# Performance work log

Measured on AMD Instinct MI355X. Metric: run time of the kernel, lower is better.

## Reference

```python
import jax, jax.numpy as jnp
import numpy as np

NUM_CLASSES = 64
BASE_MARGIN = 0.1
ADAPTIVE_WEIGHT = 0.1
STAT_WEIGHT = 0.1


def setup_inputs() -> dict:
    key = jax.random.key(0)
    k1, k2 = jax.random.split(key)
    feats = jax.random.normal(k1, (4096, 512), dtype=jnp.float32)
    labels = jax.random.randint(k2, (4096,), 0, NUM_CLASSES, dtype=jnp.int64)
    return {"feats": feats, "labels": labels}


def _forward(feats, labels):
    N, D = feats.shape
    # pairwise euclidean distances (torch.cdist p=2), nan-safe sqrt
    sq = jnp.sum(feats * feats, axis=-1)                      # [N]
    d2 = sq[:, None] + sq[None, :] - 2.0 * (feats @ feats.T)  # [N,N]
    d2 = jnp.maximum(d2, 0.0)
    dist = jnp.sqrt(jnp.where(d2 > 0.0, d2, 1.0))
    dist = jnp.where(d2 > 0.0, dist, 0.0)

    # class stats (first-call EMA == batch stats), under stop_gradient (torch.no_grad)
    sg = jax.lax.stop_gradient(feats)
    counts = jax.ops.segment_sum(jnp.ones((N,), feats.dtype), labels, NUM_CLASSES)  # [C]
    denom = jnp.maximum(counts, 1.0)[:, None]
    cmean = jax.ops.segment_sum(sg, labels, NUM_CLASSES) / denom                    # [C,D]
    cmsq = jax.ops.segment_sum(sg * sg, labels, NUM_CLASSES) / denom                # [C,D]
    cvar = jnp.maximum(cmsq - cmean * cmean, 0.0)  # biased variance (unbiased=False)

    # statistical margin per sample: ||f_i - mean[y_i]|| * mean(var[y_i])
    diff = feats - cmean[labels]                               # grads flow via feats only
    center_dist2 = jnp.sum(diff * diff, axis=-1)
    center_dist = jnp.sqrt(jnp.where(center_dist2 > 0.0, center_dist2, 1.0))
    center_dist = jnp.where(center_dist2 > 0.0, center_dist, 0.0)
    uncertainty = jnp.mean(cvar, axis=-1)[labels]              # [N]
    stat_margin = center_dist * uncertainty

    same = labels[:, None] == labels[None, :]                  # [N,N]
    eye = jnp.eye(N, dtype=bool)
    pos_mask = same & ~eye                                     # matches pos_dist > 0 filter
    neg_mask = ~same

    big = jnp.asarray(1e30, dist.dtype)
    hardest_pos = jnp.max(jnp.where(pos_mask, dist, -big), axis=1)
    hardest_neg = jnp.min(jnp.where(neg_mask, dist, big), axis=1)
    pos_cnt = jnp.sum(pos_mask, axis=1).astype(dist.dtype)
    neg_cnt = jnp.sum(neg_mask, axis=1).astype(dist.dtype)
    mean_pos = jnp.sum(jnp.where(pos_mask, dist, 0.0), axis=1) / jnp.maximum(pos_cnt, 1.0)
    mean_neg = jnp.sum(jnp.where(neg_mask, dist, 0.0), axis=1) / jnp.maximum(neg_cnt, 1.0)

    final_margin = (BASE_MARGIN + ADAPTIVE_WEIGHT * (mean_neg - mean_pos)
                    + STAT_WEIGHT * stat_margin)
    per_sample = jax.nn.relu(hardest_pos - hardest_neg + final_margin)

    valid = (pos_cnt > 0) & (neg_cnt > 0)
    n_valid = jnp.sum(valid.astype(dist.dtype))
    loss = jnp.sum(jnp.where(valid, per_sample, 0.0)) / jnp.maximum(n_valid, 1.0)
    return jnp.where(n_valid > 0, loss, 0.0)


def reference(feats, labels):
    return _forward(feats, labels)
```

## Files before the change

### kernel.cpp

```cpp
#include <hip/hip_runtime.h>
#include <hip/hip_bf16.h>


#define NN 4096
#define DD 512
#define NCLS 64

typedef __bf16 bf16x8 __attribute__((ext_vector_type(8)));
typedef float f32x4 __attribute__((ext_vector_type(4)));

__device__ __forceinline__ void gload_lds16(const void* g, void* l) {
  __builtin_amdgcn_global_load_lds(
      (const __attribute__((address_space(1))) void*)g,
      (__attribute__((address_space(3))) void*)l, 16, 0, 0);
}

__global__ __launch_bounds__(512) void k_stats(
    const float* __restrict__ feats, const int* __restrict__ labels,
    float* __restrict__ counts, float* __restrict__ cmean,
    float* __restrict__ pvar) {
  __shared__ __align__(16) int slab[NN];
  __shared__ int list[NN];
  __shared__ int chunk_off[64];
  __shared__ int sM;
  __shared__ float red1[512], red2[512];
  const int c = blockIdx.x >> 2;
  const int part = blockIdx.x & 3;
  const int t = threadIdx.x;
  const int lane = t & 63;
  const int wv = t >> 6;
  for (int i = t; i < NN; i += 512) slab[i] = labels[i];
  __syncthreads();
  for (int ch = wv; ch < 64; ch += 8) {
    const unsigned long long m = __ballot(slab[ch * 64 + lane] == c);
    if (lane == 0) chunk_off[ch] = __popcll(m);
  }
  __syncthreads();
  if (wv == 0) {
    const int v = chunk_off[lane];
    int inc = v;
#pragma unroll
    for (int off = 1; off < 64; off <<= 1) {
      const int o = __shfl_up(inc, off);
      if (lane >= off) inc += o;
    }
    chunk_off[lane] = inc - v;
    if (lane == 63) sM = inc;
  }
  __syncthreads();
  const int M = sM;
  for (int ch = wv; ch < 64; ch += 8) {
    const bool my = (slab[ch * 64 + lane] == c);
    const unsigned long long m = __ballot(my);
    if (my) {
      const int pos = chunk_off[ch] + __popcll(m & ((1ULL << lane) - 1ULL));
      list[pos] = ch * 64 + lane;
    }
  }
  __syncthreads();
  const int d = (part << 7) + (t & 127);
  const int sub = t >> 7;
  float s1 = 0.f, s2 = 0.f;
  int m = sub;
  for (; m + 16 <= M; m += 16) {
    float v[4];
#pragma unroll
    for (int e = 0; e < 4; ++e) v[e] = feats[(size_t)list[m + 4 * e] * DD + d];
#pragma unroll
    for (int e = 0; e < 4; ++e) { s1 += v[e]; s2 += v[e] * v[e]; }
  }
  for (; m < M; m += 4) {
    const float v = feats[(size_t)list[m] * DD + d];
    s1 += v; s2 += v * v;
  }
  red1[t] = s1;
  red2[t] = s2;
  __syncthreads();
  float var = 0.f;
  if (t < 128) {
    const float a1 = red1[t] + red1[t + 128] + red1[t + 256] + red1[t + 384];
    const float a2 = red2[t] + red2[t + 128] + red2[t + 256] + red2[t + 384];
    const float den = fmaxf((float)M, 1.f);
    const float mean = a1 / den;
    var = fmaxf(a2 / den - mean * mean, 0.f);
    cmean[c * DD + d] = mean;
  }
  __syncthreads();
  if (t < 128) red1[t] = var;
  __syncthreads();
  for (int s = 64; s > 0; s >>= 1) {
    if (t < s) red1[t] += red1[t + s];
    __syncthreads();
  }
  if (t == 0) {
    pvar[(c << 2) + part] = red1[0];
    if (part == 0) counts[c] = (float)M;
  }
}

__global__ __launch_bounds__(256) void k_row(
    const float* __restrict__ feats, const int* __restrict__ labels,
    const float* __restrict__ cmean, unsigned short* __restrict__ fb,
    float* __restrict__ sqb, float* __restrict__ cd2) {
  const int w = threadIdx.x >> 6;
  const int lane = threadIdx.x & 63;
  const int row = blockIdx.x * 4 + w;
  const int lab = labels[row];
  const float4* fr = (const float4*)(feats + (size_t)row * DD);
  const float4* cm = (const float4*)(cmean + (size_t)lab * DD);
  float sq = 0.f, c2 = 0.f;
  unsigned int ob[4];
#pragma unroll
  for (int h = 0; h < 2; ++h) {
    const float4 f = fr[lane * 2 + h];
    const float4 cv = cm[lane * 2 + h];
    const float fe[4] = {f.x, f.y, f.z, f.w};
    const float ce[4] = {cv.x, cv.y, cv.z, cv.w};
    unsigned short us[4];
#pragma unroll
    for (int e = 0; e < 4; ++e) {
      const __bf16 b = (__bf16)fe[e];
      const float bf = (float)b;
      sq += bf * bf;
      const float dd = fe[e] - ce[e];
      c2 += dd * dd;
      us[e] = __builtin_bit_cast(unsigned short, b);
    }
    ob[h * 2]     = (unsigned int)us[0] | ((unsigned int)us[1] << 16);
    ob[h * 2 + 1] = (unsigned int)us[2] | ((unsigned int)us[3] << 16);
  }
  *(uint4*)(fb + (size_t)row * DD + lane * 8) = make_uint4(ob[0], ob[1], ob[2], ob[3]);
#pragma unroll
  for (int off = 32; off > 0; off >>= 1) {
    sq += __shfl_xor(sq, off);
    c2 += __shfl_xor(c2, off);
  }
  if (lane == 0) {
    sqb[row] = sq;
    cd2[row] = c2;
  }
}

__global__ __launch_bounds__(512, 2) void k_gemm(
    const unsigned short* __restrict__ fb, const float* __restrict__ sqb,
    const int* __restrict__ labels,
    float* __restrict__ php, float* __restrict__ phn,
    float* __restrict__ pst, float* __restrict__ pss) {
  __shared__ __align__(16) unsigned short sA[2][256 * 64];
  __shared__ __align__(16) unsigned short sB[2][256 * 64];
  __shared__ int s_labi[256], s_labj[256];
  __shared__ float s_sqi[256], s_sqj[256];

  const int bid = blockIdx.x;
  const int xcd = bid & 7;
  const int w8 = bid >> 3;
  const int ib = ((xcd & 3) << 2) + (w8 & 3);
  const int jb = ((xcd >> 2) << 3) + (w8 >> 2);
  const int ibase = ib << 8, jbase = jb << 8;
  const int t = threadIdx.x;
  const int lane = t & 63;
  const int w = t >> 6;
  const int wm = w >> 2;
  const int wn = w & 3;
  const int rin = lane & 15;
  const int g4 = lane >> 4;
  const int swzbyte = (g4 ^ (rin & 7)) << 4;
  const int abase = ((wm << 7) + rin) << 7;
  const int bbase = ((wn << 6) + rin) << 7;

  if (t < 256) {
    s_labi[t] = labels[ibase + t];
    s_labj[t] = labels[jbase + t];
    s_sqi[t] = sqb[ibase + t];
    s_sqj[t] = sqb[jbase + t];
  }

  const unsigned short* gA[4];
  const unsigned short* gB[4];
  int lo[4];
#pragma unroll
  for (int r = 0; r < 4; ++r) {
    const int q = (r << 9) + t;
    const int row = q >> 3;
    const int ch = q & 7;
    const int koff = (ch ^ (row & 7)) << 3;
    gA[r] = fb + (size_t)(ibase + row) * DD + koff;
    gB[r] = fb + (size_t)(jbase + row) * DD + koff;
    lo[r] = q << 3;
  }

  f32x4 acc[8][4];
#pragma unroll
  for (int mi = 0; mi < 8; ++mi)
#pragma unroll
    for (int nj = 0; nj < 4; ++nj)
      acc[mi][nj] = (f32x4){0.f, 0.f, 0.f, 0.f};

#pragma unroll
  for (int r = 0; r < 4; ++r) {
    gload_lds16(gA[r], &sA[0][lo[r]]);
    gload_lds16(gB[r], &sB[0][lo[r]]);
  }

#pragma unroll
  for (int kt = 0; kt < 8; ++kt) {
    const int cur = kt & 1;
    if (kt < 7) {
#pragma unroll
      for (int r = 0; r < 4; ++r) {
        gload_lds16(gA[r] + ((kt + 1) << 6), &sA[cur ^ 1][lo[r]]);
        gload_lds16(gB[r] + ((kt + 1) << 6), &sB[cur ^ 1][lo[r]]);
      }
      asm volatile("s_waitcnt vmcnt(8)" ::: "memory");
    } else {
      asm volatile("s_waitcnt vmcnt(0)" ::: "memory");
    }
    __builtin_amdgcn_s_barrier();
    const char* A = (const char*)sA[cur];
    const char* B = (const char*)sB[cur];
#pragma unroll
    for (int ks = 0; ks < 2; ++ks) {
      bf16x8 af[8], bg[4];
#pragma unroll
      for (int mi = 0; mi < 8; ++mi)
        af[mi] = *(const bf16x8*)(A + abase + (mi << 11) + (swzbyte ^ (ks << 6)));
#pragma unroll
      for (int nj = 0; nj < 4; ++nj)
        bg[nj] = *(const bf16x8*)(B + bbase + (nj << 11) + (swzbyte ^ (ks << 6)));
#pragma unroll
      for (int mi = 0; mi < 8; ++mi)
#pragma unroll
        for (int nj = 0; nj < 4; ++nj)
          acc[mi][nj] = __builtin_amdgcn_mfma_f32_16x16x32_bf16(
              af[mi], bg[nj], acc[mi][nj], 0, 0, 0);
    }
    if (kt < 7) {
      asm volatile("s_waitcnt lgkmcnt(0)" ::: "memory");
      __builtin_amdgcn_s_barrier();
    }
  }

  float qj[4];
  int lj[4];
#pragma unroll
  for (int nj = 0; nj < 4; ++nj) {
    const int cl = (wn << 6) + (nj << 4) + rin;
    qj[nj] = s_sqj[cl];
    lj[nj] = s_labj[cl];
  }
  const int jidx = (jb << 2) + wn;
#pragma unroll
  for (int mi = 0; mi < 8; ++mi) {
#pragma unroll
    for (int r = 0; r < 4; ++r) {
      const int rl = (wm << 7) + (mi << 4) + (g4 << 2) + r;
      const float qi = s_sqi[rl];
      const int li = s_labi[rl];
      float hp = 0.f, hn = 1e30f, st = 0.f, ss = 0.f;
#pragma unroll
      for (int nj = 0; nj < 4; ++nj) {
        const float g = acc[mi][nj][r];
        float d2 = qi + qj[nj] - 2.f * g;
        d2 = fmaxf(d2, 0.f);
        const float dist = sqrtf(d2);
        const bool same = (li == lj[nj]);
        const float dp = same ? dist : 0.f;
        hp = fmaxf(hp, dp);
        hn = fminf(hn, same ? 1e30f : dist);
        st += dist;
        ss += dp;
      }
#pragma unroll
      for (int off = 1; off < 16; off <<= 1) {
        hp = fmaxf(hp, __shfl_xor(hp, off));
        hn = fminf(hn, __shfl_xor(hn, off));
        st += __shfl_xor(st, off);
        ss += __shfl_xor(ss, off);
      }
      if (rin == 0) {
        const int grow = ibase + rl;
        php[jidx * NN + grow] = hp;
        phn[jidx * NN + grow] = hn;
        pst[jidx * NN + grow] = st;
        pss[jidx * NN + grow] = ss;
      }
    }
  }
}

__global__ __launch_bounds__(1024) void k_fin1(
    const int* __restrict__ labels, const float* __restrict__ counts,
    const float* __restrict__ pvar, const float* __restrict__ cd2,
    const float* __restrict__ php, const float* __restrict__ phn,
    const float* __restrict__ pst, const float* __restrict__ pss,
    float* __restrict__ pf) {
  const int t = threadIdx.x;
  const int wv = t >> 6;
  const int lane = t & 63;
  const int row = blockIdx.x * 16 + wv;
  const size_t idx = (size_t)lane * NN + row;
  float hp = php[idx];
  float hn = phn[idx];
  float st = pst[idx];
  float ss = pss[idx];
#pragma unroll
  for (int off = 1; off < 64; off <<= 1) {
    hp = fmaxf(hp, __shfl_xor(hp, off));
    hn = fminf(hn, __shfl_xor(hn, off));
    st += __shfl_xor(st, off);
    ss += __shfl_xor(ss, off);
  }
  __shared__ float r1[16], r2[16];
  if (lane == 0) {
    const int lab = labels[row];
    const float cnt = counts[lab];
    const float pos = cnt - 1.f;
    const float neg = (float)NN - cnt;
    const float mean_pos = ss / fmaxf(pos, 1.f);
    const float mean_neg = (st - ss) / fmaxf(neg, 1.f);
    const float c2 = cd2[row];
    const float cdist = (c2 > 0.f) ? sqrtf(c2) : 0.f;
    const float uncert = (pvar[lab * 4] + pvar[lab * 4 + 1] +
                          pvar[lab * 4 + 2] + pvar[lab * 4 + 3]) * (1.f / 512.f);
    const float margin = 0.1f + 0.1f * (mean_neg - mean_pos) + 0.1f * (cdist * uncert);
    const float ps = fmaxf(hp - hn + margin, 0.f);
    const bool valid = (pos > 0.f) && (neg > 0.f);
    r1[wv] = valid ? ps : 0.f;
    r2[wv] = valid ? 1.f : 0.f;
  }
  __syncthreads();
  if (t == 0) {
    float s = 0.f, c = 0.f;
#pragma unroll
    for (int k = 0; k < 16; ++k) { s += r1[k]; c += r2[k]; }
    pf[2 * blockIdx.x] = s;
    pf[2 * blockIdx.x + 1] = c;
  }
}

__global__ __launch_bounds__(256) void k_fin2(const float* __restrict__ pf,
                                              float* __restrict__ out) {
  const int t = threadIdx.x;
  const int lane = t & 63;
  const int w = t >> 6;
  float s = pf[2 * t];
  float c = pf[2 * t + 1];
#pragma unroll
  for (int off = 1; off < 64; off <<= 1) {
    s += __shfl_xor(s, off);
    c += __shfl_xor(c, off);
  }
  __shared__ float ws1[4], ws2[4];
  if (lane == 0) { ws1[w] = s; ws2[w] = c; }
  __syncthreads();
  if (t == 0) {
    s = ws1[0] + ws1[1] + ws1[2] + ws1[3];
    c = ws2[0] + ws2[1] + ws2[2] + ws2[3];
    out[0] = (c > 0.f) ? (s / fmaxf(c, 1.f)) : 0.f;
  }
}

extern "C" void kernel_launch(void* const* d_in, const int* in_sizes, int n_in,
                              void* d_out, int out_size, void* d_ws, size_t ws_size,
                              hipStream_t stream) {
  (void)in_sizes; (void)n_in; (void)out_size; (void)ws_size;
  const float* feats = (const float*)d_in[0];
  const int* labels = (const int*)d_in[1];
  char* w = (char*)d_ws;
  float* counts = (float*)(w + 0);
  float* pvar   = (float*)(w + 1024);
  float* sqb    = (float*)(w + 2048);
  float* cd2    = (float*)(w + 18432);
  float* pf     = (float*)(w + 34816);
  float* cmean  = (float*)(w + 36864);
  unsigned short* fb = (unsigned short*)(w + 167936);
  float* php = (float*)(w + 4362240);
  float* phn = (float*)(w + 5410816);
  float* pst = (float*)(w + 6459392);
  float* pss = (float*)(w + 7507968);

  k_stats<<<dim3(256), dim3(512), 0, stream>>>(feats, labels, counts, cmean, pvar);
  k_row<<<dim3(1024), dim3(256), 0, stream>>>(feats, labels, cmean, fb, sqb, cd2);
  k_gemm<<<dim3(256), dim3(512), 0, stream>>>(fb, sqb, labels, php, phn, pst, pss);
  k_fin1<<<dim3(256), dim3(1024), 0, stream>>>(labels, counts, pvar, cd2,
                                               php, phn, pst, pss, pf);
  k_fin2<<<dim3(1), dim3(256), 0, stream>>>(pf, (float*)d_out);
}
```

Before: 58.36 us.

## Retile distance GEMM to 128x256 tiles with 4 waves and K-step 32

The pairwise-distance GEMM now uses 128x256 output tiles computed by 256-thread blocks (4 waves) instead of 256x256 tiles with 512 threads. The launch grows to 512 blocks, and the K loop runs 16 steps of 32 with a new LDS swizzle. A dummy LDS pad array is added, apparently to shape shared-memory usage and occupancy. The intent is to spread work over more blocks per CU and shrink per-block LDS. In exchange, each block reuses the B tile less and synchronises twice as often in the K loop.

New measurement: 60.56 us. 3.8% more time.

```diff
diff --git a/kernel.cpp b/kernel.cpp
--- a/kernel.cpp
+++ b/kernel.cpp
@@ -141,52 +141,61 @@
   }
 }
 
-__global__ __launch_bounds__(512, 2) void k_gemm(
+__global__ __launch_bounds__(256, 2) void k_gemm(
     const unsigned short* __restrict__ fb, const float* __restrict__ sqb,
     const int* __restrict__ labels,
     float* __restrict__ php, float* __restrict__ phn,
     float* __restrict__ pst, float* __restrict__ pss) {
-  __shared__ __align__(16) unsigned short sA[2][256 * 64];
-  __shared__ __align__(16) unsigned short sB[2][256 * 64];
-  __shared__ int s_labi[256], s_labj[256];
-  __shared__ float s_sqi[256], s_sqj[256];
+  __shared__ __align__(16) unsigned short sA[2][128 * 32];
+  __shared__ __align__(16) unsigned short sB[2][256 * 32];
+  __shared__ int s_labi[128], s_labj[256];
+  __shared__ float s_sqi[128], s_sqj[256];
+  __shared__ float s_pad[1024];
 
   const int bid = blockIdx.x;
   const int xcd = bid & 7;
   const int w8 = bid >> 3;
-  const int ib = ((xcd & 3) << 2) + (w8 & 3);
-  const int jb = ((xcd >> 2) << 3) + (w8 >> 2);
-  const int ibase = ib << 8, jbase = jb << 8;
+  const int ib = ((xcd & 3) << 3) + (w8 & 7);
+  const int jb = ((xcd >> 2) << 3) + (w8 >> 3);
+  const int ibase = ib << 7, jbase = jb << 8;
   const int t = threadIdx.x;
   const int lane = t & 63;
-  const int w = t >> 6;
-  const int wm = w >> 2;
-  const int wn = w & 3;
+  const int wn = t >> 6;
   const int rin = lane & 15;
   const int g4 = lane >> 4;
-  const int swzbyte = (g4 ^ (rin & 7)) << 4;
-  const int abase = ((wm << 7) + rin) << 7;
-  const int bbase = ((wn << 6) + rin) << 7;
-
-  if (t < 256) {
+  if (s_labj[0] == 0x7fffffff) s_pad[0] = 1.f;
+  const int koffr = (g4 ^ ((rin >> 1) & 3)) << 4;
+  const int bbase = ((wn << 6) + rin) << 6;
+
+  if (t < 128) {
     s_labi[t] = labels[ibase + t];
+    s_sqi[t] = sqb[ibase + t];
+  }
+  {
     s_labj[t] = labels[jbase + t];
-    s_sqi[t] = sqb[ibase + t];
     s_sqj[t] = sqb[jbase + t];
   }
 
-  const unsigned short* gA[4];
+  const unsigned short* gA[2];
   const unsigned short* gB[4];
-  int lo[4];
+  int loA[2], loB[4];
+#pragma unroll
+  for (int r = 0; r < 2; ++r) {
+    const int q = (r << 8) + t;
+    const int row = q >> 2;
+    const int ch = q & 3;
+    const int koff = (ch ^ ((row >> 1) & 3)) << 3;
+    gA[r] = fb + (size_t)(ibase + row) * DD + koff;
+    loA[r] = q << 3;
+  }
 #pragma unroll
   for (int r = 0; r < 4; ++r) {
-    const int q = (r << 9) + t;
-    const int row = q >> 3;
-    const int ch = q & 7;
-    const int koff = (ch ^ (row & 7)) << 3;
-    gA[r] = fb + (size_t)(ibase + row) * DD + koff;
+    const int q = (r << 8) + t;
+    const int row = q >> 2;
+    const int ch = q & 3;
+    const int koff = (ch ^ ((row >> 1) & 3)) << 3;
     gB[r] = fb + (size_t)(jbase + row) * DD + koff;
-    lo[r] = q << 3;
+    loB[r] = q << 3;
   }
 
   f32x4 acc[8][4];
@@ -197,44 +206,40 @@
       acc[mi][nj] = (f32x4){0.f, 0.f, 0.f, 0.f};
 
 #pragma unroll
-  for (int r = 0; r < 4; ++r) {
-    gload_lds16(gA[r], &sA[0][lo[r]]);
-    gload_lds16(gB[r], &sB[0][lo[r]]);
-  }
-
-#pragma unroll
-  for (int kt = 0; kt < 8; ++kt) {
+  for (int r = 0; r < 2; ++r) gload_lds16(gA[r], &sA[0][loA[r]]);
+#pragma unroll
+  for (int r = 0; r < 4; ++r) gload_lds16(gB[r], &sB[0][loB[r]]);
+
+#pragma unroll
+  for (int kt = 0; kt < 16; ++kt) {
     const int cur = kt & 1;
-    if (kt < 7) {
-#pragma unroll
-      for (int r = 0; r < 4; ++r) {
-        gload_lds16(gA[r] + ((kt + 1) << 6), &sA[cur ^ 1][lo[r]]);
-        gload_lds16(gB[r] + ((kt + 1) << 6), &sB[cur ^ 1][lo[r]]);
-      }
-      asm volatile("s_waitcnt vmcnt(8)" ::: "memory");
+    if (kt < 15) {
+      const int nk = (kt + 1) << 5;
+#pragma unroll
+      for (int r = 0; r < 2; ++r) gload_lds16(gA[r] + nk, &sA[cur ^ 1][loA[r]]);
+#pragma unroll
+      for (int r = 0; r < 4; ++r) gload_lds16(gB[r] + nk, &sB[cur ^ 1][loB[r]]);
+      asm volatile("s_waitcnt vmcnt(6)" ::: "memory");
     } else {
       asm volatile("s_waitcnt vmcnt(0)" ::: "memory");
     }
     __builtin_amdgcn_s_barrier();
     const char* A = (const char*)sA[cur];
     const char* B = (const char*)sB[cur];
-#pragma unroll
-    for (int ks = 0; ks < 2; ++ks) {
-      bf16x8 af[8], bg[4];
-#pragma unroll
-      for (int mi = 0; mi < 8; ++mi)
-        af[mi] = *(const bf16x8*)(A + abase + (mi << 11) + (swzbyte ^ (ks << 6)));
+    bf16x8 af[8], bg[4];
+#pragma unroll
+    for (int mi = 0; mi < 8; ++mi)
+      af[mi] = *(const bf16x8*)(A + (((mi << 4) + rin) << 6) + koffr);
+#pragma unroll
+    for (int nj = 0; nj < 4; ++nj)
+      bg[nj] = *(const bf16x8*)(B + bbase + (nj << 10) + koffr);
+#pragma unroll
+    for (int mi = 0; mi < 8; ++mi)
 #pragma unroll
       for (int nj = 0; nj < 4; ++nj)
-        bg[nj] = *(const bf16x8*)(B + bbase + (nj << 11) + (swzbyte ^ (ks << 6)));
-#pragma unroll
-      for (int mi = 0; mi < 8; ++mi)
-#pragma unroll
-        for (int nj = 0; nj < 4; ++nj)
-          acc[mi][nj] = __builtin_amdgcn_mfma_f32_16x16x32_bf16(
-              af[mi], bg[nj], acc[mi][nj], 0, 0, 0);
-    }
-    if (kt < 7) {
+        acc[mi][nj] = __builtin_amdgcn_mfma_f32_16x16x32_bf16(
+            af[mi], bg[nj], acc[mi][nj], 0, 0, 0);
+    if (kt < 15) {
       asm volatile("s_waitcnt lgkmcnt(0)" ::: "memory");
       __builtin_amdgcn_s_barrier();
     }
@@ -253,7 +258,7 @@
   for (int mi = 0; mi < 8; ++mi) {
 #pragma unroll
     for (int r = 0; r < 4; ++r) {
-      const int rl = (wm << 7) + (mi << 4) + (g4 << 2) + r;
+      const int rl = (mi << 4) + (g4 << 2) + r;
       const float qi = s_sqi[rl];
       const int li = s_labi[rl];
       float hp = 0.f, hn = 1e30f, st = 0.f, ss = 0.f;
@@ -381,7 +386,7 @@
 
   k_stats<<<dim3(256), dim3(512), 0, stream>>>(feats, labels, counts, cmean, pvar);
   k_row<<<dim3(1024), dim3(256), 0, stream>>>(feats, labels, cmean, fb, sqb, cd2);
-  k_gemm<<<dim3(256), dim3(512), 0, stream>>>(fb, sqb, labels, php, phn, pst, pss);
+  k_gemm<<<dim3(512), dim3(256), 0, stream>>>(fb, sqb, labels, php, phn, pst, pss);
   k_fin1<<<dim3(256), dim3(1024), 0, stream>>>(labels, counts, pvar, cd2,
                                                php, phn, pst, pss, pf);
   k_fin2<<<dim3(1), dim3(256), 0, stream>>>(pf, (float*)d_out);
```

## Merge stats and row prep kernels, move center distance to finalize, use DPP reductions

Applied to the files above, without the earlier changes.

Combines the class-statistics kernel and the bf16 row-conversion kernel into one launch with separate block roles. Because the row kernel no longer waits on class means, the feature-to-center distance is recomputed in the finalize kernel instead. The GEMM epilogue's 16-lane shuffle reductions become DPP row-rotate operations. This removes one launch and its serialization, at the cost of finalize re-reading feats and cmean.

New measurement: 54.47 us, median of 3. 6.7% less time.

```diff
diff --git a/kernel.cpp b/kernel.cpp
--- a/kernel.cpp
+++ b/kernel.cpp
@@ -15,129 +15,125 @@
       (__attribute__((address_space(3))) void*)l, 16, 0, 0);
 }
 
-__global__ __launch_bounds__(512) void k_stats(
+template <int CTRL>
+__device__ __forceinline__ float dppf(float v) {
+  return __builtin_bit_cast(float,
+      __builtin_amdgcn_update_dpp(0, __builtin_bit_cast(int, v),
+                                  CTRL, 0xf, 0xf, false));
+}
+#define ROR_STEP(CTRL)                    \
+  hp = fmaxf(hp, dppf<CTRL>(hp));         \
+  hn = fminf(hn, dppf<CTRL>(hn));         \
+  st += dppf<CTRL>(st);                   \
+  ss += dppf<CTRL>(ss);
+
+__global__ __launch_bounds__(512) void k_prep(
     const float* __restrict__ feats, const int* __restrict__ labels,
     float* __restrict__ counts, float* __restrict__ cmean,
-    float* __restrict__ pvar) {
+    float* __restrict__ pvar, unsigned short* __restrict__ fb,
+    float* __restrict__ sqb) {
   __shared__ __align__(16) int slab[NN];
   __shared__ int list[NN];
   __shared__ int chunk_off[64];
   __shared__ int sM;
   __shared__ float red1[512], red2[512];
-  const int c = blockIdx.x >> 2;
-  const int part = blockIdx.x & 3;
   const int t = threadIdx.x;
   const int lane = t & 63;
   const int wv = t >> 6;
-  for (int i = t; i < NN; i += 512) slab[i] = labels[i];
-  __syncthreads();
-  for (int ch = wv; ch < 64; ch += 8) {
-    const unsigned long long m = __ballot(slab[ch * 64 + lane] == c);
-    if (lane == 0) chunk_off[ch] = __popcll(m);
-  }
-  __syncthreads();
-  if (wv == 0) {
-    const int v = chunk_off[lane];
-    int inc = v;
-#pragma unroll
-    for (int off = 1; off < 64; off <<= 1) {
-      const int o = __shfl_up(inc, off);
-      if (lane >= off) inc += o;
-    }
-    chunk_off[lane] = inc - v;
-    if (lane == 63) sM = inc;
-  }
-  __syncthreads();
-  const int M = sM;
-  for (int ch = wv; ch < 64; ch += 8) {
-    const bool my = (slab[ch * 64 + lane] == c);
-    const unsigned long long m = __ballot(my);
-    if (my) {
-      const int pos = chunk_off[ch] + __popcll(m & ((1ULL << lane) - 1ULL));
-      list[pos] = ch * 64 + lane;
-    }
-  }
-  __syncthreads();
-  const int d = (part << 7) + (t & 127);
-  const int sub = t >> 7;
-  float s1 = 0.f, s2 = 0.f;
-  int m = sub;
-  for (; m + 16 <= M; m += 16) {
-    float v[4];
-#pragma unroll
-    for (int e = 0; e < 4; ++e) v[e] = feats[(size_t)list[m + 4 * e] * DD + d];
-#pragma unroll
-    for (int e = 0; e < 4; ++e) { s1 += v[e]; s2 += v[e] * v[e]; }
-  }
-  for (; m < M; m += 4) {
-    const float v = feats[(size_t)list[m] * DD + d];
-    s1 += v; s2 += v * v;
-  }
-  red1[t] = s1;
-  red2[t] = s2;
-  __syncthreads();
-  float var = 0.f;
-  if (t < 128) {
-    const float a1 = red1[t] + red1[t + 128] + red1[t + 256] + red1[t + 384];
-    const float a2 = red2[t] + red2[t + 128] + red2[t + 256] + red2[t + 384];
-    const float den = fmaxf((float)M, 1.f);
-    const float mean = a1 / den;
-    var = fmaxf(a2 / den - mean * mean, 0.f);
-    cmean[c * DD + d] = mean;
-  }
-  __syncthreads();
-  if (t < 128) red1[t] = var;
-  __syncthreads();
-  for (int s = 64; s > 0; s >>= 1) {
-    if (t < s) red1[t] += red1[t + s];
-    __syncthreads();
-  }
-  if (t == 0) {
-    pvar[(c << 2) + part] = red1[0];
-    if (part == 0) counts[c] = (float)M;
-  }
-}
-
-__global__ __launch_bounds__(256) void k_row(
-    const float* __restrict__ feats, const int* __restrict__ labels,
-    const float* __restrict__ cmean, unsigned short* __restrict__ fb,
-    float* __restrict__ sqb, float* __restrict__ cd2) {
-  const int w = threadIdx.x >> 6;
-  const int lane = threadIdx.x & 63;
-  const int row = blockIdx.x * 4 + w;
-  const int lab = labels[row];
-  const float4* fr = (const float4*)(feats + (size_t)row * DD);
-  const float4* cm = (const float4*)(cmean + (size_t)lab * DD);
-  float sq = 0.f, c2 = 0.f;
-  unsigned int ob[4];
-#pragma unroll
-  for (int h = 0; h < 2; ++h) {
-    const float4 f = fr[lane * 2 + h];
-    const float4 cv = cm[lane * 2 + h];
-    const float fe[4] = {f.x, f.y, f.z, f.w};
-    const float ce[4] = {cv.x, cv.y, cv.z, cv.w};
-    unsigned short us[4];
-#pragma unroll
-    for (int e = 0; e < 4; ++e) {
-      const __bf16 b = (__bf16)fe[e];
-      const float bf = (float)b;
-      sq += bf * bf;
-      const float dd = fe[e] - ce[e];
-      c2 += dd * dd;
-      us[e] = __builtin_bit_cast(unsigned short, b);
-    }
-    ob[h * 2]     = (unsigned int)us[0] | ((unsigned int)us[1] << 16);
-    ob[h * 2 + 1] = (unsigned int)us[2] | ((unsigned int)us[3] << 16);
-  }
-  *(uint4*)(fb + (size_t)row * DD + lane * 8) = make_uint4(ob[0], ob[1], ob[2], ob[3]);
-#pragma unroll
-  for (int off = 32; off > 0; off >>= 1) {
-    sq += __shfl_xor(sq, off);
-    c2 += __shfl_xor(c2, off);
-  }
-  if (lane == 0) {
-    sqb[row] = sq;
-    cd2[row] = c2;
+  if (blockIdx.x < 256) {
+    const int c = blockIdx.x >> 2;
+    const int part = blockIdx.x & 3;
+    for (int i = t; i < NN; i += 512) slab[i] = labels[i];
+    __syncthreads();
+    for (int ch = wv; ch < 64; ch += 8) {
+      const unsigned long long m = __ballot(slab[ch * 64 + lane] == c);
+      if (lane == 0) chunk_off[ch] = __popcll(m);
+    }
+    __syncthreads();
+    if (wv == 0) {
+      const int v = chunk_off[lane];
+      int inc = v;
+#pragma unroll
+      for (int off = 1; off < 64; off <<= 1) {
+        const int o = __shfl_up(inc, off);
+        if (lane >= off) inc += o;
+      }
+      chunk_off[lane] = inc - v;
+      if (lane == 63) sM = inc;
+    }
+    __syncthreads();
+    const int M = sM;
+    for (int ch = wv; ch < 64; ch += 8) {
+      const bool my = (slab[ch * 64 + lane] == c);
+      const unsigned long long m = __ballot(my);
+      if (my) {
+        const int pos = chunk_off[ch] + __popcll(m & ((1ULL << lane) - 1ULL));
+        list[pos] = ch * 64 + lane;
+      }
+    }
+    __syncthreads();
+    const int d = (part << 7) + (t & 127);
+    const int sub = t >> 7;
+    float s1 = 0.f, s2 = 0.f;
+    int m = sub;
+    for (; m + 16 <= M; m += 16) {
+      float v[4];
+#pragma unroll
+      for (int e = 0; e < 4; ++e) v[e] = feats[(size_t)list[m + 4 * e] * DD + d];
+#pragma unroll
+      for (int e = 0; e < 4; ++e) { s1 += v[e]; s2 += v[e] * v[e]; }
+    }
+    for (; m < M; m += 4) {
+      const float v = feats[(size_t)list[m] * DD + d];
+      s1 += v; s2 += v * v;
+    }
+    red1[t] = s1;
+    red2[t] = s2;
+    __syncthreads();
+    float var = 0.f;
+    if (t < 128) {
+      const float a1 = red1[t] + red1[t + 128] + red1[t + 256] + red1[t + 384];
+      const float a2 = red2[t] + red2[t + 128] + red2[t + 256] + red2[t + 384];
+      const float den = fmaxf((float)M, 1.f);
+      const float mean = a1 / den;
+      var = fmaxf(a2 / den - mean * mean, 0.f);
+      cmean[c * DD + d] = mean;
+    }
+    __syncthreads();
+    if (t < 128) red1[t] = var;
+    __syncthreads();
+    for (int s = 64; s > 0; s >>= 1) {
+      if (t < s) red1[t] += red1[t + s];
+      __syncthreads();
+    }
+    if (t == 0) {
+      pvar[(c << 2) + part] = red1[0];
+      if (part == 0) counts[c] = (float)M;
+    }
+  } else {
+    const int row = (blockIdx.x - 256) * 8 + wv;
+    const float4* fr = (const float4*)(feats + (size_t)row * DD);
+    float sq = 0.f;
+    unsigned int ob[4];
+#pragma unroll
+    for (int h = 0; h < 2; ++h) {
+      const float4 f = fr[lane * 2 + h];
+      const float fe[4] = {f.x, f.y, f.z, f.w};
+      unsigned short us[4];
+#pragma unroll
+      for (int e = 0; e < 4; ++e) {
+        const __bf16 b = (__bf16)fe[e];
+        const float bf = (float)b;
+        sq += bf * bf;
+        us[e] = __builtin_bit_cast(unsigned short, b);
+      }
+      ob[h * 2]     = (unsigned int)us[0] | ((unsigned int)us[1] << 16);
+      ob[h * 2 + 1] = (unsigned int)us[2] | ((unsigned int)us[3] << 16);
+    }
+    *(uint4*)(fb + (size_t)row * DD + lane * 8) = make_uint4(ob[0], ob[1], ob[2], ob[3]);
+#pragma unroll
+    for (int off = 32; off > 0; off >>= 1) sq += __shfl_xor(sq, off);
+    if (lane == 0) sqb[row] = sq;
   }
 }
 
@@ -270,13 +266,10 @@
         st += dist;
         ss += dp;
       }
-#pragma unroll
-      for (int off = 1; off < 16; off <<= 1) {
-        hp = fmaxf(hp, __shfl_xor(hp, off));
-        hn = fminf(hn, __shfl_xor(hn, off));
-        st += __shfl_xor(st, off);
-        ss += __shfl_xor(ss, off);
-      }
+      ROR_STEP(0x128)
+      ROR_STEP(0x124)
+      ROR_STEP(0x122)
+      ROR_STEP(0x121)
       if (rin == 0) {
         const int grow = ibase + rl;
         php[jidx * NN + grow] = hp;
@@ -290,7 +283,8 @@
 
 __global__ __launch_bounds__(1024) void k_fin1(
     const int* __restrict__ labels, const float* __restrict__ counts,
-    const float* __restrict__ pvar, const float* __restrict__ cd2,
+    const float* __restrict__ pvar, const float* __restrict__ feats,
+    const float* __restrict__ cmean,
     const float* __restrict__ php, const float* __restrict__ phn,
     const float* __restrict__ pst, const float* __restrict__ pss,
     float* __restrict__ pf) {
@@ -298,6 +292,17 @@
   const int wv = t >> 6;
   const int lane = t & 63;
   const int row = blockIdx.x * 16 + wv;
+  const int lab = labels[row];
+  const float4* fr = (const float4*)(feats + (size_t)row * DD);
+  const float4* cm = (const float4*)(cmean + (size_t)lab * DD);
+  float c2 = 0.f;
+#pragma unroll
+  for (int h = 0; h < 2; ++h) {
+    const float4 f = fr[lane * 2 + h];
+    const float4 c = cm[lane * 2 + h];
+    const float d0 = f.x - c.x, d1 = f.y - c.y, d2_ = f.z - c.z, d3 = f.w - c.w;
+    c2 += d0 * d0 + d1 * d1 + d2_ * d2_ + d3 * d3;
+  }
   const size_t idx = (size_t)lane * NN + row;
   float hp = php[idx];
   float hn = phn[idx];
@@ -309,16 +314,15 @@
     hn = fminf(hn, __shfl_xor(hn, off));
     st += __shfl_xor(st, off);
     ss += __shfl_xor(ss, off);
+    c2 += __shfl_xor(c2, off);
   }
   __shared__ float r1[16], r2[16];
   if (lane == 0) {
-    const int lab = labels[row];
     const float cnt = counts[lab];
     const float pos = cnt - 1.f;
     const float neg = (float)NN - cnt;
     const float mean_pos = ss / fmaxf(pos, 1.f);
     const float mean_neg = (st - ss) / fmaxf(neg, 1.f);
-    const float c2 = cd2[row];
     const float cdist = (c2 > 0.f) ? sqrtf(c2) : 0.f;
     const float uncert = (pvar[lab * 4] + pvar[lab * 4 + 1] +
                           pvar[lab * 4 + 2] + pvar[lab * 4 + 3]) * (1.f / 512.f);
@@ -370,7 +374,6 @@
   float* counts = (float*)(w + 0);
   float* pvar   = (float*)(w + 1024);
   float* sqb    = (float*)(w + 2048);
-  float* cd2    = (float*)(w + 18432);
   float* pf     = (float*)(w + 34816);
   float* cmean  = (float*)(w + 36864);
   unsigned short* fb = (unsigned short*)(w + 167936);
@@ -379,10 +382,10 @@
   float* pst = (float*)(w + 6459392);
   float* pss = (float*)(w + 7507968);
 
-  k_stats<<<dim3(256), dim3(512), 0, stream>>>(feats, labels, counts, cmean, pvar);
-  k_row<<<dim3(1024), dim3(256), 0, stream>>>(feats, labels, cmean, fb, sqb, cd2);
+  k_prep<<<dim3(768), dim3(512), 0, stream>>>(feats, labels, counts, cmean,
+                                              pvar, fb, sqb);
   k_gemm<<<dim3(256), dim3(512), 0, stream>>>(fb, sqb, labels, php, phn, pst, pss);
-  k_fin1<<<dim3(256), dim3(1024), 0, stream>>>(labels, counts, pvar, cd2,
-                                               php, phn, pst, pss, pf);
+  k_fin1<<<dim3(256), dim3(1024), 0, stream>>>(labels, counts, pvar, feats,
+                                               cmean, php, phn, pst, pss, pf);
   k_fin2<<<dim3(1), dim3(256), 0, stream>>>(pf, (float*)d_out);
 }
```
